# Kernel tuning notes

Measured on AMD Instinct MI355X. Metric: run time of the kernel, lower is better.

Reference implementation:

```python
import jax, jax.numpy as jnp
import numpy as np

B, T, E, NH = 2, 1024, 512, 8


def setup_inputs() -> dict:
    key = jax.random.key(0)
    ks = jax.random.split(key, 7)
    s = 0.02
    return {
        "x": jax.random.normal(ks[0], (B, T, E), dtype=jnp.float32),
        "W_qkv": jax.random.normal(ks[1], (E, 3 * E), dtype=jnp.float32) * s,
        "b_qkv": jax.random.normal(ks[2], (3 * E,), dtype=jnp.float32) * s,
        "W_od": jax.random.normal(ks[3], (E, 2 * NH), dtype=jnp.float32) * s,
        "b_od": jax.random.normal(ks[4], (2 * NH,), dtype=jnp.float32) * s,
        "W_out": jax.random.normal(ks[5], (E, E), dtype=jnp.float32) * s,
        "b_out": jax.random.normal(ks[6], (E,), dtype=jnp.float32) * s,
        "length": T,
    }


def reference(x, W_qkv, b_qkv, W_od, b_od, W_out, b_out, length):
    b, t, e = x.shape
    nh = W_od.shape[1] // 2
    hd = e // nh
    scaling = float(hd) ** (-0.5)

    qkv = x @ W_qkv + b_qkv
    Q, K, V = jnp.split(qkv, 3, axis=-1)  # each (b, t, e)

    od = Q @ W_od + b_od  # (b, t, 2*nh)
    offset, duration = jnp.split(od, 2, axis=-1)
    offset = jnp.tanh(offset) * length
    duration = jax.nn.sigmoid(duration) * length

    qidx = jnp.arange(length, dtype=x.dtype)[None, :, None]  # (1, t, 1)
    anchor = qidx + offset  # (b, t, nh)

    # 'b t nh -> (b nh) t'
    anchor = anchor.transpose(0, 2, 1).reshape(b * nh, t)
    duration = duration.transpose(0, 2, 1).reshape(b * nh, t)

    start = anchor - duration
    end = anchor + duration
    bl = jnp.floor(start)          # left bound index
    br = jnp.ceil(end)             # right bound index
    al = jnp.floor(anchor)         # anchor left index
    ar = al + 1                    # anchor right index
    dist_al = anchor - al          # anchor_dist_l

    r = jnp.arange(length, dtype=x.dtype)[None, None, :]  # (1, 1, t)

    def pmask(idx):  # point mask (bnh, t, t), float
        return (r == idx[:, :, None]).astype(x.dtype)

    point_weight = (1.0
                    + (bl - start)[:, :, None] * pmask(bl)
                    + (end - br)[:, :, None] * pmask(br)
                    + dist_al[:, :, None] * pmask(ar)
                    + (1.0 - dist_al)[:, :, None] * pmask(al))

    attn_mask = (r < bl[:, :, None]) | (r > br[:, :, None])  # (bnh, t, t) bool

    def heads(z):  # 'b t (nh hd) -> (b nh) t hd'
        return z.reshape(b, t, nh, hd).transpose(0, 2, 1, 3).reshape(b * nh, t, hd)

    Qh, Kh, Vh = heads(Q), heads(K), heads(V)

    scores = jnp.einsum('bic,brc->bir', Qh, Kh) * scaling
    scores = scores * point_weight
    scores = jnp.where(attn_mask, jnp.asarray(-1e8, x.dtype), scores)
    attn = jax.nn.softmax(scores, axis=-1)

    out = jnp.einsum('bir,brc->bic', attn, Vh)  # (bnh, t, hd)
    out = out.reshape(b, nh, t, hd).transpose(0, 2, 1, 3).reshape(b, t, e)
    return out @ W_out + b_out
```

## Files before the change

kernel.cpp:

```cpp
#include <hip/hip_runtime.h>

typedef unsigned short ushort_t;
typedef short s16x8 __attribute__((ext_vector_type(8)));
typedef short s16x4 __attribute__((ext_vector_type(4)));
typedef float f32x4 __attribute__((ext_vector_type(4)));

#if defined(__HIP_DEVICE_COMPILE__)
#define MFMA16(a, b, c) __builtin_amdgcn_mfma_f32_16x16x16bf16_1k(a, b, c, 0, 0, 0)
#else
__device__ __host__ static inline f32x4 MFMA16(s16x4, s16x4, f32x4 c) { return c; }
#endif

#define DEVINL __device__ __forceinline__

DEVINL ushort_t f2b(float f) {
  union { float f; unsigned int u; } v; v.f = f;
  unsigned int r = (v.u + 0x7fffu + ((v.u >> 16) & 1u)) >> 16;
  return (ushort_t)r;
}

DEVINL ushort_t f2b_hw(float f) {
  union { __bf16 h; ushort_t u; } cv;
  cv.h = (__bf16)f;
  return cv.u;
}

__global__ __launch_bounds__(256) void prep_kernel(
    const float* __restrict__ Wqkv, const float* __restrict__ bq,
    const float* __restrict__ Wod, const float* __restrict__ bod,
    const float* __restrict__ Wout,
    ushort_t* __restrict__ WqkvT, ushort_t* __restrict__ WoT,
    float* __restrict__ Wcomb, float* __restrict__ bcomb)
{
  __shared__ ushort_t tile[64 * 72];
  const int b = blockIdx.x;
  const int tid = threadIdx.x;

  if (b < 256) {
    const float* in;
    ushort_t* out;
    int N, bx, by;
    if (b < 192) { in = Wqkv; out = WqkvT; N = 1536; bx = b % 24; by = b / 24; }
    else         { in = Wout; out = WoT;   N = 512;  bx = (b - 192) % 8; by = (b - 192) / 8; }
    const int K = 512;
    const int n0 = bx * 64, k0 = by * 64;
    const int cr = tid >> 4;
    const int cc = (tid & 15) * 4;
#pragma unroll
    for (int p = 0; p < 4; p++) {
      int k = k0 + p * 16 + cr;
      float4 v = *(const float4*)(in + k * N + n0 + cc);
      ushort4 o; o.x = f2b(v.x); o.y = f2b(v.y); o.z = f2b(v.z); o.w = f2b(v.w);
      *(ushort4*)(tile + (p * 16 + cr) * 72 + cc) = o;
    }
    __syncthreads();
#pragma unroll
    for (int p = 0; p < 4; p++) {
      int n = n0 + p * 16 + cr;
      ushort4 v;
      v.x = tile[(cc + 0) * 72 + p * 16 + cr];
      v.y = tile[(cc + 1) * 72 + p * 16 + cr];
      v.z = tile[(cc + 2) * 72 + p * 16 + cr];
      v.w = tile[(cc + 3) * 72 + p * 16 + cr];
      *(ushort4*)(out + n * K + k0 + cc) = v;
    }
    return;
  }

  const int w = tid >> 6, lane = tid & 63;
  const int c = (b - 256) * 4 + w;
  if (c > 512) return;
  float a[8];
  const float* src = (c < 512) ? (Wqkv + c * 1536 + lane * 8) : (bq + lane * 8);
  float4 a0 = *(const float4*)(src);
  float4 a1 = *(const float4*)(src + 4);
  a[0]=a0.x; a[1]=a0.y; a[2]=a0.z; a[3]=a0.w;
  a[4]=a1.x; a[5]=a1.y; a[6]=a1.z; a[7]=a1.w;

  float s[16];
#pragma unroll
  for (int j = 0; j < 16; j++) s[j] = 0.f;
#pragma unroll
  for (int i = 0; i < 8; i++) {
    const float* wp = Wod + (lane * 8 + i) * 16;
#pragma unroll
    for (int j = 0; j < 16; j++) s[j] += a[i] * wp[j];
  }
#pragma unroll
  for (int mask = 1; mask < 64; mask <<= 1)
#pragma unroll
    for (int j = 0; j < 16; j++) s[j] += __shfl_xor(s[j], mask);

  if (lane < 16) {
    if (c < 512) Wcomb[c * 16 + lane] = s[lane];
    else         bcomb[lane] = s[lane] + bod[lane];
  }
}

__global__ __launch_bounds__(256) void qkv_od_kernel(
    const float* __restrict__ x, const ushort_t* __restrict__ WT,
    const float* __restrict__ bqkv,
    const float* __restrict__ Wcomb, const float* __restrict__ bcomb,
    const int* __restrict__ lenp,
    ushort_t* __restrict__ Qh, ushort_t* __restrict__ Kh, ushort_t* __restrict__ VT,
    float* __restrict__ params)
{
  const int blk = blockIdx.x;
  const int tid = threadIdx.x;

  if (blk >= 384) {
    const int w = tid >> 6, lane = tid & 63;
    const int m = (blk - 384) * 4 + w;
    int li = lenp[0];
    float len = (li > 0 && li < 1048576) ? (float)li : 1024.0f;

    const float* qp = x + m * 512 + lane * 8;
    float q[8];
    float4 qa = *(const float4*)(qp);
    float4 qb = *(const float4*)(qp + 4);
    q[0]=qa.x; q[1]=qa.y; q[2]=qa.z; q[3]=qa.w;
    q[4]=qb.x; q[5]=qb.y; q[6]=qb.z; q[7]=qb.w;

    float s[16];
#pragma unroll
    for (int j = 0; j < 16; j++) s[j] = 0.f;
#pragma unroll
    for (int i = 0; i < 8; i++) {
      const float* wp = Wcomb + (lane * 8 + i) * 16;
#pragma unroll
      for (int j = 0; j < 16; j++) s[j] += q[i] * wp[j];
    }
#pragma unroll
    for (int mask = 1; mask < 64; mask <<= 1)
#pragma unroll
      for (int j = 0; j < 16; j++) s[j] += __shfl_xor(s[j], mask);

    if (lane < 8) {
      int h = lane;
      int bb = m >> 10, t = m & 1023;
      float odo = s[h] + bcomb[h];
      float odd = s[8 + h] + bcomb[8 + h];
      float offset = tanhf(odo) * len;
      float dur = len / (1.f + expf(-odd));
      float anchor = (float)t + offset;
      float start = anchor - dur, end = anchor + dur;
      float bl = floorf(start), br = ceilf(end);
      float al = floorf(anchor);
      float da = anchor - al;
      float* pp = params + ((bb * 8 + h) * 1024 + t) * 6;
      pp[0] = bl; pp[1] = br; pp[2] = al;
      pp[3] = bl - start; pp[4] = end - br; pp[5] = da;
    }
    return;
  }

  __shared__ ushort_t As[64 * 32];
  __shared__ ushort_t Bs[128 * 32];
  const int lane = tid & 63, w = tid >> 6;
  const int wr = w >> 1, wc = w & 1;
  const int quad = lane >> 4, l16 = lane & 15;
  const int bx = blk % 12, by = blk / 12;
  const int m0 = by * 64, n0 = bx * 128;

  f32x4 acc[2][4];
#pragma unroll
  for (int i = 0; i < 2; i++)
#pragma unroll
    for (int j = 0; j < 4; j++) acc[i][j] = f32x4{0.f, 0.f, 0.f, 0.f};

  const int idx = tid * 8;
  const int ra = idx >> 5, ca = idx & 31;
  const int rb1 = (idx + 2048) >> 5, cb1 = (idx + 2048) & 31;

  for (int k0 = 0; k0 < 512; k0 += 32) {
    const float* xa = x + (m0 + ra) * 512 + k0 + ca;
    float4 x0 = *(const float4*)(xa);
    float4 x1 = *(const float4*)(xa + 4);
    s16x8 vb0 = *(const s16x8*)(WT + (n0 + ra) * 512 + k0 + ca);
    s16x8 vb1 = *(const s16x8*)(WT + (n0 + rb1) * 512 + k0 + cb1);
    s16x8 va;
    va[0] = (short)f2b_hw(x0.x); va[1] = (short)f2b_hw(x0.y);
    va[2] = (short)f2b_hw(x0.z); va[3] = (short)f2b_hw(x0.w);
    va[4] = (short)f2b_hw(x1.x); va[5] = (short)f2b_hw(x1.y);
    va[6] = (short)f2b_hw(x1.z); va[7] = (short)f2b_hw(x1.w);
    __syncthreads();
    *(s16x8*)(As + idx) = va;
    *(s16x8*)(Bs + idx) = vb0;
    *(s16x8*)(Bs + idx + 2048) = vb1;
    __syncthreads();

    s16x8 af[2], bfr[4];
#pragma unroll
    for (int mt = 0; mt < 2; mt++)
      af[mt] = *(const s16x8*)(As + (wr * 32 + mt * 16 + l16) * 32 + quad * 8);
#pragma unroll
    for (int nt = 0; nt < 4; nt++)
      bfr[nt] = *(const s16x8*)(Bs + (wc * 64 + nt * 16 + l16) * 32 + quad * 8);
#pragma unroll
    for (int mt = 0; mt < 2; mt++)
#pragma unroll
      for (int nt = 0; nt < 4; nt++)
        acc[mt][nt] = __builtin_amdgcn_mfma_f32_16x16x32_bf16(af[mt], bfr[nt], acc[mt][nt], 0, 0, 0);
  }

#pragma unroll
  for (int nt = 0; nt < 4; nt++) {
    int c = n0 + wc * 64 + nt * 16 + l16;
    float bias = bqkv[c];
    int which = c >> 9;
    int e = c & 511;
    int h = e >> 6, d = e & 63;
#pragma unroll
    for (int mt = 0; mt < 2; mt++) {
      int mbase = m0 + wr * 32 + mt * 16 + quad * 4;
      int bb = mbase >> 10, t = mbase & 1023;
      int bh = bb * 8 + h;
      if (which == 2) {
        ushort4 pk;
        pk.x = f2b(acc[mt][nt][0] + bias);
        pk.y = f2b(acc[mt][nt][1] + bias);
        pk.z = f2b(acc[mt][nt][2] + bias);
        pk.w = f2b(acc[mt][nt][3] + bias);
        *(ushort4*)(VT + (bh * 64 + d) * 1024 + t) = pk;
      } else {
        ushort_t* dst = (which == 0) ? Qh : Kh;
        float sc = (which == 0) ? 0.125f : 1.0f;
#pragma unroll
        for (int rr = 0; rr < 4; rr++)
          dst[(bh * 1024 + t + rr) * 64 + d] = f2b((acc[mt][nt][rr] + bias) * sc);
      }
    }
  }
}

__global__ __launch_bounds__(256, 4) void attn_kernel(
    const ushort_t* __restrict__ Qh, const ushort_t* __restrict__ Kh,
    const ushort_t* __restrict__ VT, const float* __restrict__ params,
    ushort_t* __restrict__ Oh)
{
  constexpr int TS = 64 * 72;
  __shared__ __align__(16) ushort_t KV[4 * TS];

  const int tid = threadIdx.x;
  const int lane = tid & 63, wc = tid >> 6;
  const int quad = lane >> 4, l16 = lane & 15;
  const int bh = blockIdx.x;
  const int mrow = blockIdx.y * 16;

  const float* ppl = params + (bh * 1024 + mrow + l16) * 6;
  float bl = ppl[0], br = ppl[1], al = ppl[2];
  float wl = ppl[3], wr2 = ppl[4], da = ppl[5];
  bool empty = (br < 0.f) || (bl > 1023.f);
  float lo = empty ? 0.f    : fmaxf(bl, 0.f);
  float hi = empty ? 1023.f : fminf(br, 1023.f);
#pragma unroll
  for (int mask = 1; mask < 16; mask <<= 1) {
    lo = fminf(lo, __shfl_xor(lo, mask));
    hi = fmaxf(hi, __shfl_xor(hi, mask));
  }
  const int tlo = ((int)lo) >> 6, thi = ((int)hi) >> 6;

  const ushort_t* qrow = Qh + (bh * 1024 + mrow + l16) * 64;
  s16x4 bq[4];
#pragma unroll
  for (int i = 0; i < 4; i++)
    bq[i] = *(const s16x4*)(qrow + i * 16 + quad * 4);

  float lr = 0.f;
  f32x4 Oacc[4];
#pragma unroll
  for (int g = 0; g < 4; g++) Oacc[g] = f32x4{0.f, 0.f, 0.f, 0.f};

  const int srow = tid >> 2, sseg = (tid & 3) * 16;
  const ushort_t* kgb = Kh + (bh * 1024 + srow) * 64 + sseg;
  const ushort_t* vgb = VT + (bh * 64 + srow) * 1024 + sseg;

  s16x8 kr0, kr1, vr0, vr1;
  {
    const int r0 = tlo * 64;
    kr0 = *(const s16x8*)(kgb + r0 * 64);
    kr1 = *(const s16x8*)(kgb + r0 * 64 + 8);
    vr0 = *(const s16x8*)(vgb + r0);
    vr1 = *(const s16x8*)(vgb + r0 + 8);
  }
  {
    ushort_t* Kt = KV;
    ushort_t* Vt = KV + TS;
    *(s16x8*)(Kt + srow * 72 + sseg)     = kr0;
    *(s16x8*)(Kt + srow * 72 + sseg + 8) = kr1;
    *(s16x8*)(Vt + srow * 72 + sseg)     = vr0;
    *(s16x8*)(Vt + srow * 72 + sseg + 8) = vr1;
  }
  __syncthreads();

  for (int tt = tlo; tt <= thi; tt++) {
    const int p = (tt - tlo) & 1;
    ushort_t* Ktp = KV + p * 2 * TS;
    ushort_t* Vtp = KV + p * 2 * TS + TS;
    const int r0 = tt * 64;
    const bool more = (tt + 1 <= thi);

    if (more) {
      const int r1 = (tt + 1) * 64;
      kr0 = *(const s16x8*)(kgb + r1 * 64);
      kr1 = *(const s16x8*)(kgb + r1 * 64 + 8);
      vr0 = *(const s16x8*)(vgb + r1);
      vr1 = *(const s16x8*)(vgb + r1 + 8);
    }

    const ushort_t* krow = Ktp + (wc * 16 + l16) * 72;
    f32x4 z = {0.f, 0.f, 0.f, 0.f};
#pragma unroll
    for (int i = 0; i < 4; i++) {
      s16x4 ak = *(const s16x4*)(krow + i * 16 + quad * 4);
      z = MFMA16(ak, bq[i], z);
    }

    const int cbase = r0 + wc * 16;
    const float c0f = (float)cbase, c1f = c0f + 15.f;
    bool f = (bl < c0f) && (br > c1f) && ((al + 1.f < c0f) || (al > c1f));
    s16x4 pt;
    if (__all((int)f)) {
#pragma unroll
      for (int rr = 0; rr < 4; rr++) {
        float pv = __expf(z[rr]);
        lr += pv;
        pt[rr] = (short)f2b_hw(pv);
      }
    } else {
#pragma unroll
      for (int rr = 0; rr < 4; rr++) {
        float cf = (float)(cbase + quad * 4 + rr);
        float s = z[rr];
        float wgt = 1.f;
        wgt += (cf == bl) ? wl : 0.f;
        wgt += (cf == br) ? wr2 : 0.f;
        wgt += (cf == al + 1.f) ? da : 0.f;
        wgt += (cf == al) ? (1.f - da) : 0.f;
        s *= wgt;
        s = (cf < bl || cf > br) ? -30.f : s;
        float pv = __expf(s);
        lr += pv;
        pt[rr] = (short)f2b_hw(pv);
      }
    }

#pragma unroll
    for (int g = 0; g < 4; g++) {
      s16x4 av = *(const s16x4*)(Vtp + (g * 16 + l16) * 72 + wc * 16 + quad * 4);
      Oacc[g] = MFMA16(av, pt, Oacc[g]);
    }

    if (more) {
      ushort_t* Ktn = KV + (p ^ 1) * 2 * TS;
      ushort_t* Vtn = KV + (p ^ 1) * 2 * TS + TS;
      *(s16x8*)(Ktn + srow * 72 + sseg)     = kr0;
      *(s16x8*)(Ktn + srow * 72 + sseg + 8) = kr1;
      *(s16x8*)(Vtn + srow * 72 + sseg)     = vr0;
      *(s16x8*)(Vtn + srow * 72 + sseg + 8) = vr1;
      __syncthreads();
    }
  }

  lr += __shfl_xor(lr, 16);
  lr += __shfl_xor(lr, 32);

  __syncthreads();
  float* Om  = (float*)KV;
  float* lwf = Om + 64 * 65;
#pragma unroll
  for (int g = 0; g < 4; g++)
#pragma unroll
    for (int rr = 0; rr < 4; rr++)
      Om[(wc * 16 + l16) * 65 + g * 16 + quad * 4 + rr] = Oacc[g][rr];
  if (quad == 0) lwf[wc * 16 + l16] = lr;
  __syncthreads();

  const int bb = bh >> 3, h = bh & 7;
  {
    int e = tid;
#pragma unroll
    for (int it = 0; it < 4; it++, e += 256) {
      int r = e >> 6, col = e & 63;
      float lg = lwf[r] + lwf[16 + r] + lwf[32 + r] + lwf[48 + r];
      float o  = Om[r * 65 + col] + Om[(16 + r) * 65 + col]
               + Om[(32 + r) * 65 + col] + Om[(48 + r) * 65 + col];
      int t = mrow + r;
      Oh[((bb << 10) + t) * 512 + h * 64 + col] = f2b_hw(o / lg);
    }
  }
}

__global__ __launch_bounds__(256) void out_gemm_kernel(
    const ushort_t* __restrict__ Oh, const ushort_t* __restrict__ WT,
    const float* __restrict__ bout, float* __restrict__ outp)
{
  __shared__ ushort_t As[64 * 32];
  __shared__ ushort_t Bs[64 * 32];
  const int tid = threadIdx.x;
  const int lane = tid & 63, w = tid >> 6;
  const int wr = w >> 1, wc = w & 1;
  const int quad = lane >> 4, l16 = lane & 15;
  const int m0 = blockIdx.y * 64, n0 = blockIdx.x * 64;

  f32x4 acc[2][2];
#pragma unroll
  for (int i = 0; i < 2; i++)
#pragma unroll
    for (int j = 0; j < 2; j++) acc[i][j] = f32x4{0.f, 0.f, 0.f, 0.f};

  const int idx = tid * 8;
  const int ra = idx >> 5, ca = idx & 31;

  for (int k0 = 0; k0 < 512; k0 += 32) {
    s16x8 va = *(const s16x8*)(Oh + (m0 + ra) * 512 + k0 + ca);
    s16x8 vb = *(const s16x8*)(WT + (n0 + ra) * 512 + k0 + ca);
    __syncthreads();
    *(s16x8*)(As + idx) = va;
    *(s16x8*)(Bs + idx) = vb;
    __syncthreads();

    s16x8 af[2], bfr[2];
#pragma unroll
    for (int mt = 0; mt < 2; mt++)
      af[mt] = *(const s16x8*)(As + (wr * 32 + mt * 16 + l16) * 32 + quad * 8);
#pragma unroll
    for (int nt = 0; nt < 2; nt++)
      bfr[nt] = *(const s16x8*)(Bs + (wc * 32 + nt * 16 + l16) * 32 + quad * 8);
#pragma unroll
    for (int mt = 0; mt < 2; mt++)
#pragma unroll
      for (int nt = 0; nt < 2; nt++)
        acc[mt][nt] = __builtin_amdgcn_mfma_f32_16x16x32_bf16(af[mt], bfr[nt], acc[mt][nt], 0, 0, 0);
  }

#pragma unroll
  for (int nt = 0; nt < 2; nt++) {
    int c = n0 + wc * 32 + nt * 16 + l16;
    float bias = bout[c];
#pragma unroll
    for (int mt = 0; mt < 2; mt++) {
#pragma unroll
      for (int rr = 0; rr < 4; rr++) {
        int m = m0 + wr * 32 + mt * 16 + quad * 4 + rr;
        outp[m * 512 + c] = acc[mt][nt][rr] + bias;
      }
    }
  }
}

extern "C" void kernel_launch(void* const* d_in, const int* in_sizes, int n_in,
                              void* d_out, int out_size, void* d_ws, size_t ws_size,
                              hipStream_t stream)
{
  const float* x    = (const float*)d_in[0];
  const float* Wqkv = (const float*)d_in[1];
  const float* bqkv = (const float*)d_in[2];
  const float* Wod  = (const float*)d_in[3];
  const float* bod  = (const float*)d_in[4];
  const float* Wout = (const float*)d_in[5];
  const float* bout = (const float*)d_in[6];
  const int* lenp   = (const int*)d_in[7];

  char* ws = (char*)d_ws;
  ushort_t* WqkvT  = (ushort_t*)(ws);
  ushort_t* WoT    = (ushort_t*)(ws + 1572864);
  ushort_t* Qh     = (ushort_t*)(ws + 4194304);
  ushort_t* Kh     = (ushort_t*)(ws + 6291456);
  ushort_t* VT     = (ushort_t*)(ws + 8388608);
  ushort_t* Oh     = (ushort_t*)(ws + 10485760);
  float*    Wcomb  = (float*)(ws + 12582912);
  float*    bcomb  = (float*)(ws + 12615680);
  float*    params = (float*)(ws + 12615744);

  prep_kernel<<<385, 256, 0, stream>>>(Wqkv, bqkv, Wod, bod, Wout, WqkvT, WoT, Wcomb, bcomb);
  qkv_od_kernel<<<896, 256, 0, stream>>>(x, WqkvT, bqkv, Wcomb, bcomb, lenp,
                                         Qh, Kh, VT, params);
  attn_kernel<<<dim3(16, 64), 256, 0, stream>>>(Qh, Kh, VT, params, Oh);
  out_gemm_kernel<<<dim3(8, 32), 256, 0, stream>>>(Oh, WoT, bout, (float*)d_out);
}
```

Baseline: 126.6 us.

## Split attention KV tiles across two 256-thread groups per block

The attention block grows to 512 threads. Each half processes alternating 64-key tiles into its own LDS buffer, and the partial outputs and row sums of all 8 waves are reduced at the end. This replaces the single-group double-buffered prefetch loop with a two-way parallel split over key tiles, aiming to shorten the serial tile chain per query block. It also adds s_setprio around the MFMA sections and readfirstlane on the tile bounds. In exchange, register-prefetch overlap is lost, there are two barriers per iteration, and one group may idle when the tile count is odd.

```diff
diff --git a/kernel.cpp b/kernel.cpp
--- a/kernel.cpp
+++ b/kernel.cpp
@@ -233,7 +233,7 @@
   }
 }
 
-__global__ __launch_bounds__(256, 4) void attn_kernel(
+__global__ __launch_bounds__(512, 6) void attn_kernel(
     const ushort_t* __restrict__ Qh, const ushort_t* __restrict__ Kh,
     const ushort_t* __restrict__ VT, const float* __restrict__ params,
     ushort_t* __restrict__ Oh)
@@ -242,7 +242,10 @@
   __shared__ __align__(16) ushort_t KV[4 * TS];
 
   const int tid = threadIdx.x;
-  const int lane = tid & 63, wc = tid >> 6;
+  const int wg = tid >> 8;
+  const int t8 = tid & 255;
+  const int lane = tid & 63;
+  const int wc = t8 >> 6;
   const int quad = lane >> 4, l16 = lane & 15;
   const int bh = blockIdx.x;
   const int mrow = blockIdx.y * 16;
@@ -258,7 +261,10 @@
     lo = fminf(lo, __shfl_xor(lo, mask));
     hi = fmaxf(hi, __shfl_xor(hi, mask));
   }
-  const int tlo = ((int)lo) >> 6, thi = ((int)hi) >> 6;
+  const int tlo = __builtin_amdgcn_readfirstlane(((int)lo) >> 6);
+  const int thi = __builtin_amdgcn_readfirstlane(((int)hi) >> 6);
+  const int ntile = thi - tlo + 1;
+  const int iters = (ntile + 1) >> 1;
 
   const ushort_t* qrow = Qh + (bh * 1024 + mrow + l16) * 64;
   s16x4 bq[4];
@@ -271,50 +277,44 @@
 #pragma unroll
   for (int g = 0; g < 4; g++) Oacc[g] = f32x4{0.f, 0.f, 0.f, 0.f};
 
-  const int srow = tid >> 2, sseg = (tid & 3) * 16;
+  const int srow = t8 >> 2, sseg = (t8 & 3) * 16;
   const ushort_t* kgb = Kh + (bh * 1024 + srow) * 64 + sseg;
   const ushort_t* vgb = VT + (bh * 64 + srow) * 1024 + sseg;
-
-  s16x8 kr0, kr1, vr0, vr1;
-  {
-    const int r0 = tlo * 64;
-    kr0 = *(const s16x8*)(kgb + r0 * 64);
-    kr1 = *(const s16x8*)(kgb + r0 * 64 + 8);
-    vr0 = *(const s16x8*)(vgb + r0);
-    vr1 = *(const s16x8*)(vgb + r0 + 8);
-  }
-  {
-    ushort_t* Kt = KV;
-    ushort_t* Vt = KV + TS;
-    *(s16x8*)(Kt + srow * 72 + sseg)     = kr0;
-    *(s16x8*)(Kt + srow * 72 + sseg + 8) = kr1;
-    *(s16x8*)(Vt + srow * 72 + sseg)     = vr0;
-    *(s16x8*)(Vt + srow * 72 + sseg + 8) = vr1;
-  }
-  __syncthreads();
-
-  for (int tt = tlo; tt <= thi; tt++) {
-    const int p = (tt - tlo) & 1;
-    ushort_t* Ktp = KV + p * 2 * TS;
-    ushort_t* Vtp = KV + p * 2 * TS + TS;
+  ushort_t* Kt = KV + wg * 2 * TS;
+  ushort_t* Vt = Kt + TS;
+
+  for (int i = 0; i < iters; i++) {
+    const int ti = 2 * i + wg;
+    const bool act = (ti < ntile);
+    const int tt = tlo + ti;
     const int r0 = tt * 64;
-    const bool more = (tt + 1 <= thi);
-
-    if (more) {
-      const int r1 = (tt + 1) * 64;
-      kr0 = *(const s16x8*)(kgb + r1 * 64);
-      kr1 = *(const s16x8*)(kgb + r1 * 64 + 8);
-      vr0 = *(const s16x8*)(vgb + r1);
-      vr1 = *(const s16x8*)(vgb + r1 + 8);
-    }
-
-    const ushort_t* krow = Ktp + (wc * 16 + l16) * 72;
+
+    s16x8 kr0, kr1, vr0, vr1;
+    if (act) {
+      kr0 = *(const s16x8*)(kgb + r0 * 64);
+      kr1 = *(const s16x8*)(kgb + r0 * 64 + 8);
+      vr0 = *(const s16x8*)(vgb + r0);
+      vr1 = *(const s16x8*)(vgb + r0 + 8);
+    }
+    __syncthreads();
+    if (act) {
+      *(s16x8*)(Kt + srow * 72 + sseg)     = kr0;
+      *(s16x8*)(Kt + srow * 72 + sseg + 8) = kr1;
+      *(s16x8*)(Vt + srow * 72 + sseg)     = vr0;
+      *(s16x8*)(Vt + srow * 72 + sseg + 8) = vr1;
+    }
+    __syncthreads();
+    if (!act) continue;
+
+    const ushort_t* krow = Kt + (wc * 16 + l16) * 72;
     f32x4 z = {0.f, 0.f, 0.f, 0.f};
-#pragma unroll
-    for (int i = 0; i < 4; i++) {
-      s16x4 ak = *(const s16x4*)(krow + i * 16 + quad * 4);
-      z = MFMA16(ak, bq[i], z);
-    }
+    __builtin_amdgcn_s_setprio(1);
+#pragma unroll
+    for (int ii = 0; ii < 4; ii++) {
+      s16x4 ak = *(const s16x4*)(krow + ii * 16 + quad * 4);
+      z = MFMA16(ak, bq[ii], z);
+    }
+    __builtin_amdgcn_s_setprio(0);
 
     const int cbase = r0 + wc * 16;
     const float c0f = (float)cbase, c1f = c0f + 15.f;
@@ -345,21 +345,13 @@
       }
     }
 
+    __builtin_amdgcn_s_setprio(1);
 #pragma unroll
     for (int g = 0; g < 4; g++) {
-      s16x4 av = *(const s16x4*)(Vtp + (g * 16 + l16) * 72 + wc * 16 + quad * 4);
+      s16x4 av = *(const s16x4*)(Vt + (g * 16 + l16) * 72 + wc * 16 + quad * 4);
       Oacc[g] = MFMA16(av, pt, Oacc[g]);
     }
-
-    if (more) {
-      ushort_t* Ktn = KV + (p ^ 1) * 2 * TS;
-      ushort_t* Vtn = KV + (p ^ 1) * 2 * TS + TS;
-      *(s16x8*)(Ktn + srow * 72 + sseg)     = kr0;
-      *(s16x8*)(Ktn + srow * 72 + sseg + 8) = kr1;
-      *(s16x8*)(Vtn + srow * 72 + sseg)     = vr0;
-      *(s16x8*)(Vtn + srow * 72 + sseg + 8) = vr1;
-      __syncthreads();
-    }
+    __builtin_amdgcn_s_setprio(0);
   }
 
   lr += __shfl_xor(lr, 16);
@@ -367,24 +359,28 @@
 
   __syncthreads();
   float* Om  = (float*)KV;
-  float* lwf = Om + 64 * 65;
+  float* lwf = Om + 128 * 65;
+  const int prow = (wg * 4 + wc) * 16 + l16;
 #pragma unroll
   for (int g = 0; g < 4; g++)
 #pragma unroll
     for (int rr = 0; rr < 4; rr++)
-      Om[(wc * 16 + l16) * 65 + g * 16 + quad * 4 + rr] = Oacc[g][rr];
-  if (quad == 0) lwf[wc * 16 + l16] = lr;
+      Om[prow * 65 + g * 16 + quad * 4 + rr] = Oacc[g][rr];
+  if (quad == 0) lwf[prow] = lr;
   __syncthreads();
 
   const int bb = bh >> 3, h = bh & 7;
   {
     int e = tid;
 #pragma unroll
-    for (int it = 0; it < 4; it++, e += 256) {
+    for (int it = 0; it < 2; it++, e += 512) {
       int r = e >> 6, col = e & 63;
-      float lg = lwf[r] + lwf[16 + r] + lwf[32 + r] + lwf[48 + r];
-      float o  = Om[r * 65 + col] + Om[(16 + r) * 65 + col]
-               + Om[(32 + r) * 65 + col] + Om[(48 + r) * 65 + col];
+      float lg = 0.f, o = 0.f;
+#pragma unroll
+      for (int p = 0; p < 8; p++) {
+        lg += lwf[p * 16 + r];
+        o  += Om[(p * 16 + r) * 65 + col];
+      }
       int t = mrow + r;
       Oh[((bb << 10) + t) * 512 + h * 64 + col] = f2b_hw(o / lg);
     }
@@ -476,6 +472,6 @@
   prep_kernel<<<385, 256, 0, stream>>>(Wqkv, bqkv, Wod, bod, Wout, WqkvT, WoT, Wcomb, bcomb);
   qkv_od_kernel<<<896, 256, 0, stream>>>(x, WqkvT, bqkv, Wcomb, bcomb, lenp,
                                          Qh, Kh, VT, params);
-  attn_kernel<<<dim3(16, 64), 256, 0, stream>>>(Qh, Kh, VT, params, Oh);
+  attn_kernel<<<dim3(16, 64), 512, 0, stream>>>(Qh, Kh, VT, params, Oh);
   out_gemm_kernel<<<dim3(8, 32), 256, 0, stream>>>(Oh, WoT, bout, (float*)d_out);
 }
```

Result: slower. 131.2 us (+3.7%).

## Load K/V fragments directly from global into registers, dropping LDS staging

Applied to the files above, without the earlier changes.

The attention kernel no longer stages K and V tiles through double-buffered shared memory with block barriers. Each wave now loads its MFMA operands straight from global memory (relying on L1/L2 for reuse), and QK^T uses the 16x16x32 bf16 MFMA so it needs two instructions instead of four. MFMA sections are wrapped in s_setprio, and the launch-bounds occupancy hint is removed. This removes per-tile barriers and LDS traffic, but adds exposed global-load latency with no prefetch and redundant global reads across waves.

```diff
diff --git a/kernel.cpp b/kernel.cpp
--- a/kernel.cpp
+++ b/kernel.cpp
@@ -10,6 +10,7 @@
 #else
 __device__ __host__ static inline f32x4 MFMA16(s16x4, s16x4, f32x4 c) { return c; }
 #endif
+#define MFMA32(a, b, c) __builtin_amdgcn_mfma_f32_16x16x32_bf16(a, b, c, 0, 0, 0)
 
 #define DEVINL __device__ __forceinline__
 
@@ -233,14 +234,12 @@
   }
 }
 
-__global__ __launch_bounds__(256, 4) void attn_kernel(
+__global__ __launch_bounds__(256) void attn_kernel(
     const ushort_t* __restrict__ Qh, const ushort_t* __restrict__ Kh,
     const ushort_t* __restrict__ VT, const float* __restrict__ params,
     ushort_t* __restrict__ Oh)
 {
-  constexpr int TS = 64 * 72;
-  __shared__ __align__(16) ushort_t KV[4 * TS];
-
+  __shared__ __align__(16) float Om[64 * 65 + 64];
   const int tid = threadIdx.x;
   const int lane = tid & 63, wc = tid >> 6;
   const int quad = lane >> 4, l16 = lane & 15;
@@ -261,60 +260,32 @@
   const int tlo = ((int)lo) >> 6, thi = ((int)hi) >> 6;
 
   const ushort_t* qrow = Qh + (bh * 1024 + mrow + l16) * 64;
-  s16x4 bq[4];
-#pragma unroll
-  for (int i = 0; i < 4; i++)
-    bq[i] = *(const s16x4*)(qrow + i * 16 + quad * 4);
+  s16x8 bq0 = *(const s16x8*)(qrow + quad * 8);
+  s16x8 bq1 = *(const s16x8*)(qrow + 32 + quad * 8);
 
   float lr = 0.f;
   f32x4 Oacc[4];
 #pragma unroll
   for (int g = 0; g < 4; g++) Oacc[g] = f32x4{0.f, 0.f, 0.f, 0.f};
 
-  const int srow = tid >> 2, sseg = (tid & 3) * 16;
-  const ushort_t* kgb = Kh + (bh * 1024 + srow) * 64 + sseg;
-  const ushort_t* vgb = VT + (bh * 64 + srow) * 1024 + sseg;
-
-  s16x8 kr0, kr1, vr0, vr1;
-  {
-    const int r0 = tlo * 64;
-    kr0 = *(const s16x8*)(kgb + r0 * 64);
-    kr1 = *(const s16x8*)(kgb + r0 * 64 + 8);
-    vr0 = *(const s16x8*)(vgb + r0);
-    vr1 = *(const s16x8*)(vgb + r0 + 8);
-  }
-  {
-    ushort_t* Kt = KV;
-    ushort_t* Vt = KV + TS;
-    *(s16x8*)(Kt + srow * 72 + sseg)     = kr0;
-    *(s16x8*)(Kt + srow * 72 + sseg + 8) = kr1;
-    *(s16x8*)(Vt + srow * 72 + sseg)     = vr0;
-    *(s16x8*)(Vt + srow * 72 + sseg + 8) = vr1;
-  }
-  __syncthreads();
+  const ushort_t* kbase = Kh + (bh * 1024 + wc * 16 + l16) * 64 + quad * 8;
+  const ushort_t* vbase = VT + (bh * 64 + l16) * 1024 + wc * 16 + quad * 4;
 
   for (int tt = tlo; tt <= thi; tt++) {
-    const int p = (tt - tlo) & 1;
-    ushort_t* Ktp = KV + p * 2 * TS;
-    ushort_t* Vtp = KV + p * 2 * TS + TS;
     const int r0 = tt * 64;
-    const bool more = (tt + 1 <= thi);
-
-    if (more) {
-      const int r1 = (tt + 1) * 64;
-      kr0 = *(const s16x8*)(kgb + r1 * 64);
-      kr1 = *(const s16x8*)(kgb + r1 * 64 + 8);
-      vr0 = *(const s16x8*)(vgb + r1);
-      vr1 = *(const s16x8*)(vgb + r1 + 8);
-    }
-
-    const ushort_t* krow = Ktp + (wc * 16 + l16) * 72;
+
+    s16x8 ak0 = *(const s16x8*)(kbase + r0 * 64);
+    s16x8 ak1 = *(const s16x8*)(kbase + r0 * 64 + 32);
+    s16x4 av0 = *(const s16x4*)(vbase + r0);
+    s16x4 av1 = *(const s16x4*)(vbase + r0 + 16384);
+    s16x4 av2 = *(const s16x4*)(vbase + r0 + 32768);
+    s16x4 av3 = *(const s16x4*)(vbase + r0 + 49152);
+
     f32x4 z = {0.f, 0.f, 0.f, 0.f};
-#pragma unroll
-    for (int i = 0; i < 4; i++) {
-      s16x4 ak = *(const s16x4*)(krow + i * 16 + quad * 4);
-      z = MFMA16(ak, bq[i], z);
-    }
+    __builtin_amdgcn_s_setprio(1);
+    z = MFMA32(ak0, bq0, z);
+    z = MFMA32(ak1, bq1, z);
+    __builtin_amdgcn_s_setprio(0);
 
     const int cbase = r0 + wc * 16;
     const float c0f = (float)cbase, c1f = c0f + 15.f;
@@ -345,28 +316,17 @@
       }
     }
 
-#pragma unroll
-    for (int g = 0; g < 4; g++) {
-      s16x4 av = *(const s16x4*)(Vtp + (g * 16 + l16) * 72 + wc * 16 + quad * 4);
-      Oacc[g] = MFMA16(av, pt, Oacc[g]);
-    }
-
-    if (more) {
-      ushort_t* Ktn = KV + (p ^ 1) * 2 * TS;
-      ushort_t* Vtn = KV + (p ^ 1) * 2 * TS + TS;
-      *(s16x8*)(Ktn + srow * 72 + sseg)     = kr0;
-      *(s16x8*)(Ktn + srow * 72 + sseg + 8) = kr1;
-      *(s16x8*)(Vtn + srow * 72 + sseg)     = vr0;
-      *(s16x8*)(Vtn + srow * 72 + sseg + 8) = vr1;
-      __syncthreads();
-    }
+    __builtin_amdgcn_s_setprio(1);
+    Oacc[0] = MFMA16(av0, pt, Oacc[0]);
+    Oacc[1] = MFMA16(av1, pt, Oacc[1]);
+    Oacc[2] = MFMA16(av2, pt, Oacc[2]);
+    Oacc[3] = MFMA16(av3, pt, Oacc[3]);
+    __builtin_amdgcn_s_setprio(0);
   }
 
   lr += __shfl_xor(lr, 16);
   lr += __shfl_xor(lr, 32);
 
-  __syncthreads();
-  float* Om  = (float*)KV;
   float* lwf = Om + 64 * 65;
 #pragma unroll
   for (int g = 0; g < 4; g++)
```

New measurement: 150.3 us. +18.8%, slower.

## Pre-convert x to bf16 and stage GEMM tiles via direct global-to-LDS loads

Applied to the files above, without the earlier changes.

Adds a bf16 copy of x, produced by extra blocks in the prep kernel, so the QKV GEMM no longer converts fp32 to bf16 inside its K loop. Both the QKV GEMM and the output GEMM now fill shared memory with global_load_lds 16-byte transfers instead of loading into registers and then storing to LDS. This is meant to cut register traffic and instruction count in the main loops. In exchange it adds an extra write and read pass over x in the workspace, and it depends on the per-wave LDS address layout matching the old tile layout.

```diff
diff --git a/kernel.cpp b/kernel.cpp
--- a/kernel.cpp
+++ b/kernel.cpp
@@ -13,6 +13,14 @@
 
 #define DEVINL __device__ __forceinline__
 
+DEVINL void gload_lds16(const void* g, void* l) {
+#if defined(__HIP_DEVICE_COMPILE__)
+  __builtin_amdgcn_global_load_lds((const __attribute__((address_space(1))) void*)g,
+                                   (__attribute__((address_space(3))) void*)l,
+                                   16, 0, 0);
+#endif
+}
+
 DEVINL ushort_t f2b(float f) {
   union { float f; unsigned int u; } v; v.f = f;
   unsigned int r = (v.u + 0x7fffu + ((v.u >> 16) & 1u)) >> 16;
@@ -28,9 +36,10 @@
 __global__ __launch_bounds__(256) void prep_kernel(
     const float* __restrict__ Wqkv, const float* __restrict__ bq,
     const float* __restrict__ Wod, const float* __restrict__ bod,
-    const float* __restrict__ Wout,
+    const float* __restrict__ Wout, const float* __restrict__ x,
     ushort_t* __restrict__ WqkvT, ushort_t* __restrict__ WoT,
-    float* __restrict__ Wcomb, float* __restrict__ bcomb)
+    float* __restrict__ Wcomb, float* __restrict__ bcomb,
+    ushort_t* __restrict__ xbf)
 {
   __shared__ ushort_t tile[64 * 72];
   const int b = blockIdx.x;
@@ -67,6 +76,19 @@
     return;
   }
 
+  if (b >= 385) {
+    const int base = (b - 385) * 2048 + tid * 8;
+    float4 v0 = *(const float4*)(x + base);
+    float4 v1 = *(const float4*)(x + base + 4);
+    s16x8 o;
+    o[0] = (short)f2b_hw(v0.x); o[1] = (short)f2b_hw(v0.y);
+    o[2] = (short)f2b_hw(v0.z); o[3] = (short)f2b_hw(v0.w);
+    o[4] = (short)f2b_hw(v1.x); o[5] = (short)f2b_hw(v1.y);
+    o[6] = (short)f2b_hw(v1.z); o[7] = (short)f2b_hw(v1.w);
+    *(s16x8*)(xbf + base) = o;
+    return;
+  }
+
   const int w = tid >> 6, lane = tid & 63;
   const int c = (b - 256) * 4 + w;
   if (c > 512) return;
@@ -98,7 +120,8 @@
 }
 
 __global__ __launch_bounds__(256) void qkv_od_kernel(
-    const float* __restrict__ x, const ushort_t* __restrict__ WT,
+    const float* __restrict__ x, const ushort_t* __restrict__ xbf,
+    const ushort_t* __restrict__ WT,
     const float* __restrict__ bqkv,
     const float* __restrict__ Wcomb, const float* __restrict__ bcomb,
     const int* __restrict__ lenp,
@@ -154,8 +177,8 @@
     return;
   }
 
-  __shared__ ushort_t As[64 * 32];
-  __shared__ ushort_t Bs[128 * 32];
+  __shared__ __align__(16) ushort_t As[64 * 32];
+  __shared__ __align__(16) ushort_t Bs[128 * 32];
   const int lane = tid & 63, w = tid >> 6;
   const int wr = w >> 1, wc = w & 1;
   const int quad = lane >> 4, l16 = lane & 15;
@@ -171,22 +194,19 @@
   const int idx = tid * 8;
   const int ra = idx >> 5, ca = idx & 31;
   const int rb1 = (idx + 2048) >> 5, cb1 = (idx + 2048) & 31;
+  const int wbase = w << 10;
+  char* asb  = (char*)As + wbase;
+  char* bsb0 = (char*)Bs + wbase;
+  char* bsb1 = (char*)Bs + 4096 + wbase;
+  const ushort_t* ga  = xbf + (m0 + ra) * 512 + ca;
+  const ushort_t* gb0 = WT + (n0 + ra) * 512 + ca;
+  const ushort_t* gb1 = WT + (n0 + rb1) * 512 + cb1;
 
   for (int k0 = 0; k0 < 512; k0 += 32) {
-    const float* xa = x + (m0 + ra) * 512 + k0 + ca;
-    float4 x0 = *(const float4*)(xa);
-    float4 x1 = *(const float4*)(xa + 4);
-    s16x8 vb0 = *(const s16x8*)(WT + (n0 + ra) * 512 + k0 + ca);
-    s16x8 vb1 = *(const s16x8*)(WT + (n0 + rb1) * 512 + k0 + cb1);
-    s16x8 va;
-    va[0] = (short)f2b_hw(x0.x); va[1] = (short)f2b_hw(x0.y);
-    va[2] = (short)f2b_hw(x0.z); va[3] = (short)f2b_hw(x0.w);
-    va[4] = (short)f2b_hw(x1.x); va[5] = (short)f2b_hw(x1.y);
-    va[6] = (short)f2b_hw(x1.z); va[7] = (short)f2b_hw(x1.w);
     __syncthreads();
-    *(s16x8*)(As + idx) = va;
-    *(s16x8*)(Bs + idx) = vb0;
-    *(s16x8*)(Bs + idx + 2048) = vb1;
+    gload_lds16(ga + k0, asb);
+    gload_lds16(gb0 + k0, bsb0);
+    gload_lds16(gb1 + k0, bsb1);
     __syncthreads();
 
     s16x8 af[2], bfr[4];
@@ -395,8 +415,8 @@
     const ushort_t* __restrict__ Oh, const ushort_t* __restrict__ WT,
     const float* __restrict__ bout, float* __restrict__ outp)
 {
-  __shared__ ushort_t As[64 * 32];
-  __shared__ ushort_t Bs[64 * 32];
+  __shared__ __align__(16) ushort_t As[64 * 32];
+  __shared__ __align__(16) ushort_t Bs[64 * 32];
   const int tid = threadIdx.x;
   const int lane = tid & 63, w = tid >> 6;
   const int wr = w >> 1, wc = w & 1;
@@ -411,13 +431,16 @@
 
   const int idx = tid * 8;
   const int ra = idx >> 5, ca = idx & 31;
+  const int wbase = w << 10;
+  char* asb = (char*)As + wbase;
+  char* bsb = (char*)Bs + wbase;
+  const ushort_t* ga = Oh + (m0 + ra) * 512 + ca;
+  const ushort_t* gb = WT + (n0 + ra) * 512 + ca;
 
   for (int k0 = 0; k0 < 512; k0 += 32) {
-    s16x8 va = *(const s16x8*)(Oh + (m0 + ra) * 512 + k0 + ca);
-    s16x8 vb = *(const s16x8*)(WT + (n0 + ra) * 512 + k0 + ca);
     __syncthreads();
-    *(s16x8*)(As + idx) = va;
-    *(s16x8*)(Bs + idx) = vb;
+    gload_lds16(ga + k0, asb);
+    gload_lds16(gb + k0, bsb);
     __syncthreads();
 
     s16x8 af[2], bfr[2];
@@ -472,9 +495,11 @@
   float*    Wcomb  = (float*)(ws + 12582912);
   float*    bcomb  = (float*)(ws + 12615680);
   float*    params = (float*)(ws + 12615744);
-
-  prep_kernel<<<385, 256, 0, stream>>>(Wqkv, bqkv, Wod, bod, Wout, WqkvT, WoT, Wcomb, bcomb);
-  qkv_od_kernel<<<896, 256, 0, stream>>>(x, WqkvT, bqkv, Wcomb, bcomb, lenp,
+  ushort_t* xbf    = (ushort_t*)(ws + 13008960);
+
+  prep_kernel<<<897, 256, 0, stream>>>(Wqkv, bqkv, Wod, bod, Wout, x,
+                                       WqkvT, WoT, Wcomb, bcomb, xbf);
+  qkv_od_kernel<<<896, 256, 0, stream>>>(x, xbf, WqkvT, bqkv, Wcomb, bcomb, lenp,
                                          Qh, Kh, VT, params);
   attn_kernel<<<dim3(16, 64), 256, 0, stream>>>(Qh, Kh, VT, params, Oh);
   out_gemm_kernel<<<dim3(8, 32), 256, 0, stream>>>(Oh, WoT, bout, (float*)d_out);
```

After: 124.4 us. No clear change (-1.7%).
